# Kernel tuning notes

Measured on AMD Instinct MI355X. Metric: run time of the kernel, lower is better.

## Reference

```python
import jax, jax.numpy as jnp
import numpy as np

N, D_IN, D_ATTN = 8192, 48, 8


def setup_inputs() -> dict:
    key = jax.random.key(0)
    ks = jax.random.split(key, 9)
    s = 1.0 / np.sqrt(D_IN)
    return {
        "x": jax.random.normal(ks[0], (N, D_IN), jnp.float32),
        "Kw": jax.random.normal(ks[1], (D_IN, D_ATTN), jnp.float32) * s,
        "Kb": jax.random.normal(ks[2], (D_ATTN,), jnp.float32) * s,
        "Qw": jax.random.normal(ks[3], (D_IN, D_ATTN), jnp.float32) * s,
        "Qb": jax.random.normal(ks[4], (D_ATTN,), jnp.float32) * s,
        "Vw": jax.random.normal(ks[5], (D_IN, D_ATTN), jnp.float32) * s,
        "Vb": jax.random.normal(ks[6], (D_ATTN,), jnp.float32) * s,
        "Zw": jax.random.normal(ks[7], (D_ATTN, D_IN), jnp.float32) * (1.0 / np.sqrt(D_ATTN)),
        "Zb": jax.random.normal(ks[8], (D_IN,), jnp.float32) * (1.0 / np.sqrt(D_ATTN)),
    }


def reference(x, Kw, Kb, Qw, Qb, Vw, Vb, Zw, Zb):
    # Tiny QKV projections: [N,48] -> [N,8]
    Xk = x @ Kw + Kb
    Xq = x @ Qw + Qb
    Xv = x @ Vw + Vb
    # Attention over the batch/row dimension: [N,8]@[8,N] -> [N,N]
    scale = jnp.sqrt(jnp.asarray(D_ATTN, jnp.float32))
    AM = jax.nn.softmax(Xk @ Xq.T / scale, axis=1)  # torch F.softmax 2D default dim=1
    Z = AM @ Xv                                      # [N,8]
    return x + (Z @ Zw + Zb)                         # residual + output proj [N,48]
```

## Files before the change

kernel.cpp:

```cpp
#include <hip/hip_runtime.h>
#include <hip/hip_fp16.h>


#define QV_OFF   32768
#define BMAX_OFF 98304
#define PART_OFF 98560

typedef _Float16 hv2 __attribute__((ext_vector_type(2)));
union HVU { unsigned u; hv2 v; };

static __device__ __forceinline__ unsigned pku(float a, float b) {
    auto t = __builtin_amdgcn_cvt_pkrtz(a, b);
    union { decltype(t) x; unsigned u; } c; c.x = t; return c.u;
}
static __device__ __forceinline__ hv2 asV(unsigned u) { HVU t; t.u = u; return t.v; }
static __device__ __forceinline__ hv2 h2fma(hv2 a, hv2 b, hv2 c) {
#if __has_builtin(__builtin_elementwise_fma)
    return __builtin_elementwise_fma(a, b, c);
#else
    union { hv2 v; __half2 h; } A, B, C, D;
    A.v = a; B.v = b; C.v = c;
    D.h = __hfma2(A.h, B.h, C.h);
    return D.v;
#endif
}
static __device__ __forceinline__ unsigned dupL(unsigned u) {
    const unsigned lo = u & 0xFFFFu; return lo | (lo << 16);
}
static __device__ __forceinline__ unsigned dupH(unsigned u) {
    const unsigned hi = u >> 16; return hi | (hi << 16);
}

__global__ __launch_bounds__(256) void proj_kernel(
    const float* __restrict__ x,
    const float* __restrict__ Kw, const float* __restrict__ Kb,
    const float* __restrict__ Qw, const float* __restrict__ Qb,
    const float* __restrict__ Vw, const float* __restrict__ Vb,
    unsigned* __restrict__ Xksf16, unsigned* __restrict__ QV,
    float* __restrict__ bmax)
{
    __shared__ float xs[32 * 49];
    __shared__ float wAll[3 * 388];
    __shared__ float bs[24];
    __shared__ float outv[32][25];
    const int tid = threadIdx.x;
    const int r0 = blockIdx.x * 32;

    for (int i = tid; i < 1536; i += 256) {
        int r = i / 48, c = i - r * 48;
        xs[r * 49 + c] = x[r0 * 48 + i];
    }
    for (int i = tid; i < 384; i += 256) {
        wAll[i]       = Kw[i];
        wAll[388 + i] = Qw[i];
        wAll[776 + i] = Vw[i];
    }
    if (tid < 8)       bs[tid] = Kb[tid];
    else if (tid < 16) bs[tid] = Qb[tid - 8];
    else if (tid < 24) bs[tid] = Vb[tid - 16];
    __syncthreads();

    const int rl = tid >> 3;
    const int g  = tid & 7;
    const int c0 = 3 * g;
    const float* xr = &xs[rl * 49];
    const float* w0 = &wAll[((c0 + 0) >> 3) * 388 + ((c0 + 0) & 7)];
    const float* w1 = &wAll[((c0 + 1) >> 3) * 388 + ((c0 + 1) & 7)];
    const float* w2 = &wAll[((c0 + 2) >> 3) * 388 + ((c0 + 2) & 7)];
    float a0 = bs[c0], a1 = bs[c0 + 1], a2 = bs[c0 + 2];
    #pragma unroll
    for (int k = 0; k < 48; k++) {
        const float xv = xr[k];
        a0 = fmaf(xv, w0[k * 8], a0);
        a1 = fmaf(xv, w1[k * 8], a1);
        a2 = fmaf(xv, w2[k * 8], a2);
    }
    outv[rl][c0] = a0; outv[rl][c0 + 1] = a1; outv[rl][c0 + 2] = a2;
    __syncthreads();

    {
        const int p = tid >> 4;
        const int c = (tid >> 1) & 7;
        const int m = tid & 1;
        const int col = (m ? 16 : 8) + c;
        QV[(blockIdx.x * 16 + p) * 16 + m * 8 + c] =
            pku(outv[2 * p][col], outv[2 * p + 1][col]);
    }
    const float kscale = 0.51008732149f;
    if (tid < 32) {
        uint4 o;
        o.x = pku(outv[tid][0] * kscale, outv[tid][1] * kscale);
        o.y = pku(outv[tid][2] * kscale, outv[tid][3] * kscale);
        o.z = pku(outv[tid][4] * kscale, outv[tid][5] * kscale);
        o.w = pku(outv[tid][6] * kscale, outv[tid][7] * kscale);
        ((uint4*)Xksf16)[r0 + tid] = o;
    }
    if (tid >= 192 && tid < 224) {
        const int r = tid - 192;
        float n2 = 0.f;
        #pragma unroll
        for (int c = 0; c < 8; c++) n2 = fmaf(outv[r][8 + c], outv[r][8 + c], n2);
        #pragma unroll
        for (int off = 16; off > 0; off >>= 1)
            n2 = fmaxf(n2, __shfl_xor(n2, off, 64));
        if (r == 0) bmax[blockIdx.x] = n2;
    }
}

__global__ __launch_bounds__(256) void attn_kernel(
    const unsigned* __restrict__ Xksf16, const unsigned* __restrict__ QV,
    const float* __restrict__ bmax,
    float* __restrict__ part, int ppw)
{
    __shared__ float red[4][64][13];
    const int tid  = threadIdx.x;
    const int lane = tid & 63;
    const int wv   = tid >> 6;
    const int rgrp  = blockIdx.x & 127;
    const int chunk = blockIdx.x >> 7;
    const int row   = rgrp * 64 + lane;

    float m = fmaxf(fmaxf(bmax[lane], bmax[64 + lane]),
                    fmaxf(bmax[128 + lane], bmax[192 + lane]));
    #pragma unroll
    for (int off = 32; off > 0; off >>= 1)
        m = fmaxf(m, __shfl_xor(m, off, 64));
    const float qmax2 = m;

    const uint4 kv = ((const uint4*)Xksf16)[row];
    unsigned kd[8];
    kd[0] = dupL(kv.x); kd[1] = dupH(kv.x);
    kd[2] = dupL(kv.y); kd[3] = dupH(kv.y);
    kd[4] = dupL(kv.z); kd[5] = dupH(kv.z);
    kd[6] = dupL(kv.w); kd[7] = dupH(kv.w);
    float kn2 = 0.f;
    #pragma unroll
    for (int c = 0; c < 8; c++) {
        const float kf = (float)asV(kd[c]).x;
        kn2 = fmaf(kf, kf, kn2);
    }
    const float sinit = -sqrtf(kn2 * qmax2);
    const hv2 sinit2 = asV(pku(sinit, sinit));
    const hv2 one2   = asV(0x3C003C00u);
    hv2 l2 = asV(0u), acc[8];
    #pragma unroll
    for (int c = 0; c < 8; c++) acc[c] = asV(0u);

    const int pbase = __builtin_amdgcn_readfirstlane((chunk * 4 + wv) * ppw);
    const uint4* QV4 = (const uint4*)QV + (size_t)pbase * 4;

    #pragma unroll 4
    for (int p = 0; p < ppw; p++) {
        const uint4 qp0 = QV4[p * 4 + 0];
        const uint4 qp1 = QV4[p * 4 + 1];
        const uint4 vp0 = QV4[p * 4 + 2];
        const uint4 vp1 = QV4[p * 4 + 3];
        hv2 s2 = sinit2;
        s2 = h2fma(asV(kd[0]), asV(qp0.x), s2);
        s2 = h2fma(asV(kd[1]), asV(qp0.y), s2);
        s2 = h2fma(asV(kd[2]), asV(qp0.z), s2);
        s2 = h2fma(asV(kd[3]), asV(qp0.w), s2);
        s2 = h2fma(asV(kd[4]), asV(qp1.x), s2);
        s2 = h2fma(asV(kd[5]), asV(qp1.y), s2);
        s2 = h2fma(asV(kd[6]), asV(qp1.z), s2);
        s2 = h2fma(asV(kd[7]), asV(qp1.w), s2);
        const float pa = __builtin_amdgcn_exp2f((float)s2.x);
        const float pb = __builtin_amdgcn_exp2f((float)s2.y);
        const hv2 ph = asV(pku(pa, pb));
        l2 = h2fma(ph, one2, l2);
        acc[0] = h2fma(ph, asV(vp0.x), acc[0]);
        acc[1] = h2fma(ph, asV(vp0.y), acc[1]);
        acc[2] = h2fma(ph, asV(vp0.z), acc[2]);
        acc[3] = h2fma(ph, asV(vp0.w), acc[3]);
        acc[4] = h2fma(ph, asV(vp1.x), acc[4]);
        acc[5] = h2fma(ph, asV(vp1.y), acc[5]);
        acc[6] = h2fma(ph, asV(vp1.z), acc[6]);
        acc[7] = h2fma(ph, asV(vp1.w), acc[7]);
    }

    #pragma unroll
    for (int c = 0; c < 8; c++)
        red[wv][lane][c] = (float)acc[c].x + (float)acc[c].y;
    red[wv][lane][8] = (float)l2.x + (float)l2.y;
    __syncthreads();
    for (int e = tid; e < 576; e += 256) {
        const int r = e / 9, c = e - r * 9;
        const float s = red[0][r][c] + red[1][r][c] + red[2][r][c] + red[3][r][c];
        part[((size_t)chunk * 8192 + rgrp * 64 + r) * 9 + c] = s;
    }
}

__global__ __launch_bounds__(256) void finish_kernel(
    const float* __restrict__ x,
    const float* __restrict__ Zw, const float* __restrict__ Zb,
    const float* __restrict__ part, float* __restrict__ out, int nch)
{
    __shared__ float Zs[128 * 9];
    __shared__ float zw_s[384];
    __shared__ float zb_s[48];
    const int tid = threadIdx.x;
    const int r0 = blockIdx.x * 128;

    for (int i = tid; i < 384; i += 256) zw_s[i] = Zw[i];
    if (tid < 48) zb_s[tid] = Zb[tid];

    if (tid < 128) {
        const int row = r0 + tid;
        float a[9];
        #pragma unroll
        for (int c = 0; c < 9; c++) a[c] = 0.f;
        for (int ch = 0; ch < nch; ch++) {
            const float* p = part + ((size_t)ch * 8192 + row) * 9;
            #pragma unroll
            for (int c = 0; c < 9; c++) a[c] += p[c];
        }
        const float inv = 1.0f / a[8];
        #pragma unroll
        for (int c = 0; c < 8; c++) Zs[tid * 9 + c] = a[c] * inv;
    }
    __syncthreads();

    for (int e = tid; e < 128 * 48; e += 256) {
        const int r = e / 48, c = e - r * 48;
        float o = x[r0 * 48 + e] + zb_s[c];
        #pragma unroll
        for (int k = 0; k < 8; k++) o = fmaf(Zs[r * 9 + k], zw_s[k * 48 + c], o);
        out[r0 * 48 + e] = o;
    }
}

extern "C" void kernel_launch(void* const* d_in, const int* in_sizes, int n_in,
                              void* d_out, int out_size, void* d_ws, size_t ws_size,
                              hipStream_t stream) {
    const float* x  = (const float*)d_in[0];
    const float* Kw = (const float*)d_in[1];
    const float* Kb = (const float*)d_in[2];
    const float* Qw = (const float*)d_in[3];
    const float* Qb = (const float*)d_in[4];
    const float* Vw = (const float*)d_in[5];
    const float* Vb = (const float*)d_in[6];
    const float* Zw = (const float*)d_in[7];
    const float* Zb = (const float*)d_in[8];
    float* out = (float*)d_out;

    float* ws = (float*)d_ws;
    unsigned* Xksf16 = (unsigned*)ws;
    unsigned* QV     = (unsigned*)(ws + QV_OFF);
    float* bmax      = ws + BMAX_OFF;
    float* part      = ws + PART_OFF;

    int nch = 16;
    const size_t avail = ws_size / 4;
    while (nch > 1 && (size_t)PART_OFF + (size_t)nch * 8192 * 9 > avail) nch >>= 1;
    const int ppw = 1024 / nch;

    proj_kernel<<<256, 256, 0, stream>>>(x, Kw, Kb, Qw, Qb, Vw, Vb,
                                         Xksf16, QV, bmax);
    attn_kernel<<<128 * nch, 256, 0, stream>>>(Xksf16, QV, bmax, part, ppw);
    finish_kernel<<<64, 256, 0, stream>>>(x, Zw, Zb, part, out, nch);
}
```

Before: 115.5 us.

## Stage QV chunk tile in LDS and use inline v_pk_fma_f16 in attention loop

```diff
diff --git a/kernel.cpp b/kernel.cpp
--- a/kernel.cpp
+++ b/kernel.cpp
@@ -14,21 +14,14 @@
     union { decltype(t) x; unsigned u; } c; c.x = t; return c.u;
 }
 static __device__ __forceinline__ hv2 asV(unsigned u) { HVU t; t.u = u; return t.v; }
-static __device__ __forceinline__ hv2 h2fma(hv2 a, hv2 b, hv2 c) {
-#if __has_builtin(__builtin_elementwise_fma)
-    return __builtin_elementwise_fma(a, b, c);
-#else
-    union { hv2 v; __half2 h; } A, B, C, D;
-    A.v = a; B.v = b; C.v = c;
-    D.h = __hfma2(A.h, B.h, C.h);
-    return D.v;
-#endif
-}
 static __device__ __forceinline__ unsigned dupL(unsigned u) {
     const unsigned lo = u & 0xFFFFu; return lo | (lo << 16);
 }
 static __device__ __forceinline__ unsigned dupH(unsigned u) {
     const unsigned hi = u >> 16; return hi | (hi << 16);
+}
+static __device__ __forceinline__ void pkfma(unsigned& d, unsigned a, unsigned b) {
+    asm("v_pk_fma_f16 %0, %1, %2, %0" : "+v"(d) : "v"(a), "v"(b));
 }
 
 __global__ __launch_bounds__(256) void proj_kernel(
@@ -112,13 +105,20 @@
     const float* __restrict__ bmax,
     float* __restrict__ part, int ppw)
 {
-    __shared__ float red[4][64][13];
+    extern __shared__ char smem[];
+    uint4* tile4 = (uint4*)smem;
+    float (*red)[64][13] = (float (*)[64][13])smem;
+
     const int tid  = threadIdx.x;
     const int lane = tid & 63;
     const int wv   = tid >> 6;
     const int rgrp  = blockIdx.x & 127;
     const int chunk = blockIdx.x >> 7;
     const int row   = rgrp * 64 + lane;
+    const int npair = 4 * ppw;
+
+    for (int i = tid; i < npair * 4; i += 256)
+        tile4[i] = ((const uint4*)QV)[(size_t)chunk * npair * 4 + i];
 
     float m = fmaxf(fmaxf(bmax[lane], bmax[64 + lane]),
                     fmaxf(bmax[128 + lane], bmax[192 + lane]));
@@ -140,48 +140,56 @@
         kn2 = fmaf(kf, kf, kn2);
     }
     const float sinit = -sqrtf(kn2 * qmax2);
-    const hv2 sinit2 = asV(pku(sinit, sinit));
-    const hv2 one2   = asV(0x3C003C00u);
-    hv2 l2 = asV(0u), acc[8];
-    #pragma unroll
-    for (int c = 0; c < 8; c++) acc[c] = asV(0u);
-
-    const int pbase = __builtin_amdgcn_readfirstlane((chunk * 4 + wv) * ppw);
-    const uint4* QV4 = (const uint4*)QV + (size_t)pbase * 4;
-
+    const unsigned sinit2 = pku(sinit, sinit);
+    const unsigned one2 = 0x3C003C00u;
+    unsigned l2 = 0u, acc[8];
+    #pragma unroll
+    for (int c = 0; c < 8; c++) acc[c] = 0u;
+
+    __syncthreads();
+
+    const uint4* tw = tile4 + (size_t)wv * ppw * 4;
     #pragma unroll 4
     for (int p = 0; p < ppw; p++) {
-        const uint4 qp0 = QV4[p * 4 + 0];
-        const uint4 qp1 = QV4[p * 4 + 1];
-        const uint4 vp0 = QV4[p * 4 + 2];
-        const uint4 vp1 = QV4[p * 4 + 3];
-        hv2 s2 = sinit2;
-        s2 = h2fma(asV(kd[0]), asV(qp0.x), s2);
-        s2 = h2fma(asV(kd[1]), asV(qp0.y), s2);
-        s2 = h2fma(asV(kd[2]), asV(qp0.z), s2);
-        s2 = h2fma(asV(kd[3]), asV(qp0.w), s2);
-        s2 = h2fma(asV(kd[4]), asV(qp1.x), s2);
-        s2 = h2fma(asV(kd[5]), asV(qp1.y), s2);
-        s2 = h2fma(asV(kd[6]), asV(qp1.z), s2);
-        s2 = h2fma(asV(kd[7]), asV(qp1.w), s2);
-        const float pa = __builtin_amdgcn_exp2f((float)s2.x);
-        const float pb = __builtin_amdgcn_exp2f((float)s2.y);
-        const hv2 ph = asV(pku(pa, pb));
-        l2 = h2fma(ph, one2, l2);
-        acc[0] = h2fma(ph, asV(vp0.x), acc[0]);
-        acc[1] = h2fma(ph, asV(vp0.y), acc[1]);
-        acc[2] = h2fma(ph, asV(vp0.z), acc[2]);
-        acc[3] = h2fma(ph, asV(vp0.w), acc[3]);
-        acc[4] = h2fma(ph, asV(vp1.x), acc[4]);
-        acc[5] = h2fma(ph, asV(vp1.y), acc[5]);
-        acc[6] = h2fma(ph, asV(vp1.z), acc[6]);
-        acc[7] = h2fma(ph, asV(vp1.w), acc[7]);
-    }
-
-    #pragma unroll
-    for (int c = 0; c < 8; c++)
-        red[wv][lane][c] = (float)acc[c].x + (float)acc[c].y;
-    red[wv][lane][8] = (float)l2.x + (float)l2.y;
+        const uint4 qp0 = tw[p * 4 + 0];
+        const uint4 qp1 = tw[p * 4 + 1];
+        const uint4 vp0 = tw[p * 4 + 2];
+        const uint4 vp1 = tw[p * 4 + 3];
+        unsigned s2 = sinit2;
+        pkfma(s2, kd[0], qp0.x);
+        pkfma(s2, kd[1], qp0.y);
+        pkfma(s2, kd[2], qp0.z);
+        pkfma(s2, kd[3], qp0.w);
+        pkfma(s2, kd[4], qp1.x);
+        pkfma(s2, kd[5], qp1.y);
+        pkfma(s2, kd[6], qp1.z);
+        pkfma(s2, kd[7], qp1.w);
+        const hv2 s2v = asV(s2);
+        const float pa = __builtin_amdgcn_exp2f((float)s2v.x);
+        const float pb = __builtin_amdgcn_exp2f((float)s2v.y);
+        const unsigned ph = pku(pa, pb);
+        pkfma(l2, ph, one2);
+        pkfma(acc[0], ph, vp0.x);
+        pkfma(acc[1], ph, vp0.y);
+        pkfma(acc[2], ph, vp0.z);
+        pkfma(acc[3], ph, vp0.w);
+        pkfma(acc[4], ph, vp1.x);
+        pkfma(acc[5], ph, vp1.y);
+        pkfma(acc[6], ph, vp1.z);
+        pkfma(acc[7], ph, vp1.w);
+    }
+
+    __syncthreads();
+
+    #pragma unroll
+    for (int c = 0; c < 8; c++) {
+        const hv2 a = asV(acc[c]);
+        red[wv][lane][c] = (float)a.x + (float)a.y;
+    }
+    {
+        const hv2 lv = asV(l2);
+        red[wv][lane][8] = (float)lv.x + (float)lv.y;
+    }
     __syncthreads();
     for (int e = tid; e < 576; e += 256) {
         const int r = e / 9, c = e - r * 9;
@@ -254,8 +262,12 @@
     while (nch > 1 && (size_t)PART_OFF + (size_t)nch * 8192 * 9 > avail) nch >>= 1;
     const int ppw = 1024 / nch;
 
+    const int tile_bytes = 4 * ppw * 64;
+    const int smem_bytes = tile_bytes > 13312 ? tile_bytes : 13312;
+
     proj_kernel<<<256, 256, 0, stream>>>(x, Kw, Kb, Qw, Qb, Vw, Vb,
                                          Xksf16, QV, bmax);
-    attn_kernel<<<128 * nch, 256, 0, stream>>>(Xksf16, QV, bmax, part, ppw);
+    attn_kernel<<<128 * nch, 256, smem_bytes, stream>>>(Xksf16, QV, bmax,
+                                                        part, ppw);
     finish_kernel<<<64, 256, 0, stream>>>(x, Zw, Zb, part, out, nch);
 }
```

Measured after the change: 117.6 us. Within noise of the previous version (+1.8%).
